# Kernel optimization log

Measured on AMD Instinct MI355X. Metric: run time of the kernel, lower is better.

The kernel has to match this reference:

```python
import jax, jax.numpy as jnp
import numpy as np

LAMBDA_SOFTMAX = 9.0
LAMBDA_LSE = 6.0
MARGIN = 0.2
EPS = 1e-8


def setup_inputs() -> dict:
    key = jax.random.key(0)
    k1, k2 = jax.random.split(key)
    im = jax.random.normal(k1, (128, 36, 1024), dtype=jnp.float32)
    s = jax.random.normal(k2, (128, 32, 1024), dtype=jnp.float32)
    return {"im": im, "s": s}


def _xattn_scores_t2i(im, s):
    # im: (n_image=J, n_region=R, D); s: (n_caption=I, n_word=W, D)
    # raw attention: context(image regions) x query(caption words)
    attn = jnp.einsum('jrd,iwd->ijrw', im, s)              # (I,J,R,W)
    # clipped_l2norm: LeakyReLU(0.1) then L2-normalize over word axis (dim=2 of (B,R,W))
    attn = jnp.where(attn > 0, attn, 0.1 * attn)
    norm = jnp.sqrt(jnp.sum(attn * attn, axis=3, keepdims=True)) + EPS
    attn = attn / norm
    # transpose to (I,J,W,R), softmax over regions with smoothing
    attn = jax.nn.softmax(LAMBDA_SOFTMAX * jnp.swapaxes(attn, 2, 3), axis=3)
    # weighted context per word: (I,J,W,D)
    wctx = jnp.einsum('ijwr,jrd->ijwd', attn, im)
    # cosine similarity between caption words and weighted image context, over D
    num = jnp.einsum('iwd,ijwd->ijw', s, wctx)
    w1 = jnp.linalg.norm(s, axis=2)                        # (I,W)
    w2 = jnp.linalg.norm(wctx, axis=3)                     # (I,J,W)
    sim = num / jnp.clip(w1[:, None, :] * w2, EPS, None)   # (I,J,W)
    # LogSumExp aggregation over words
    row = jax.nn.logsumexp(LAMBDA_LSE * sim, axis=2) / LAMBDA_LSE  # (I,J)
    # original stacks row_sim (n_image,1) along dim=1 -> scores[j, i]
    return row.T                                           # (n_image, n_caption)


def reference(im, s):
    scores = _xattn_scores_t2i(im, s)                      # (B,B)
    diag = jnp.diagonal(scores)
    cost_s = jnp.clip(MARGIN + scores - diag[:, None], 0.0, None)
    cost_im = jnp.clip(MARGIN + scores - diag[None, :], 0.0, None)
    mask = jnp.eye(scores.shape[0], dtype=bool)
    cost_s = jnp.where(mask, 0.0, cost_s)
    cost_im = jnp.where(mask, 0.0, cost_im)
    # max_violation = True
    return jnp.max(cost_s, axis=1).sum() + jnp.max(cost_im, axis=0).sum()
```

## Files before the change

### kernel.cpp

```cpp
#include <hip/hip_runtime.h>

#define NJ 128
#define NI 128
#define NR 36
#define NW 32
#define ND 1024

#define LAM_SM 9.0f
#define LAM_LSE 6.0f
#define MARGIN 0.2f
#define EPSF 1e-8f

typedef __attribute__((ext_vector_type(8))) short s16x8;
typedef __attribute__((ext_vector_type(4))) float f32x4;

#define IM_ROWS (NJ * NR)
#define S_ROWS  (NI * NW)
#define ALL_ROWS (IM_ROWS + S_ROWS)
#define IM_ELEMS (IM_ROWS * ND)
#define S_ELEMS  (S_ROWS * ND)
#define GSW_ELEMS (NJ * 48 * 64)

#define G_BOFF 36864
#define G_BUFSZ 69632
#define G_SMEM 139264
#define GRAM_SMEM 98304

__device__ __forceinline__ unsigned short f2bf(float x) {
    unsigned u = __float_as_uint(x);
    return (unsigned short)((u + 0x7FFFu + ((u >> 16) & 1u)) >> 16);
}
__device__ __forceinline__ unsigned pack2bf(float x, float y) {
    return (unsigned)f2bf(x) | ((unsigned)f2bf(y) << 16);
}
__device__ __forceinline__ float bf2f(unsigned v) {
    return __uint_as_float((v & 0xffffu) << 16);
}
__device__ __forceinline__ void gload16(const void* g, void* l) {
    __builtin_amdgcn_global_load_lds((const __attribute__((address_space(1))) unsigned int*)g,
                                     (__attribute__((address_space(3))) unsigned int*)l, 16, 0, 0);
}

__global__ __launch_bounds__(256) void cvtswz2_kernel(const float* __restrict__ im,
                                                      const float* __restrict__ s,
                                                      unsigned short* __restrict__ dst,
                                                      float* __restrict__ w1) {
    __shared__ float part[4];
    const int tid = threadIdx.x;
    int idx = blockIdx.x * 256 + tid;
    int row = idx >> 7, cw = idx & 127;
    int wd = cw >> 3, p = cw & 7;
    int sk = wd * 64 + ((p ^ (row & 7)) * 8);
    const float* srow = (row < IM_ROWS) ? (im + (size_t)row * ND)
                                        : (s + (size_t)(row - IM_ROWS) * ND);
    float4 v0 = *(const float4*)(srow + sk);
    float4 v1 = *(const float4*)(srow + sk + 4);
    ushort4 o0, o1;
    o0.x = f2bf(v0.x); o0.y = f2bf(v0.y); o0.z = f2bf(v0.z); o0.w = f2bf(v0.w);
    o1.x = f2bf(v1.x); o1.y = f2bf(v1.y); o1.z = f2bf(v1.z); o1.w = f2bf(v1.w);
    ((ushort4*)dst)[(size_t)idx * 2] = o0;
    ((ushort4*)dst)[(size_t)idx * 2 + 1] = o1;
    float ss = v0.x * v0.x + v0.y * v0.y + v0.z * v0.z + v0.w * v0.w +
               v1.x * v1.x + v1.y * v1.y + v1.z * v1.z + v1.w * v1.w;
    ss += __shfl_xor(ss, 1);  ss += __shfl_xor(ss, 2);  ss += __shfl_xor(ss, 4);
    ss += __shfl_xor(ss, 8);  ss += __shfl_xor(ss, 16); ss += __shfl_xor(ss, 32);
    if ((tid & 63) == 0) part[tid >> 6] = ss;
    __syncthreads();
    if ((tid & 127) == 0 && row >= IM_ROWS) {
        int h = tid >> 7;
        w1[row - IM_ROWS] = sqrtf(part[h * 2] + part[h * 2 + 1]);
    }
}

__global__ __launch_bounds__(512) void gram4_kernel(const unsigned short* __restrict__ imsw,
                                                    unsigned short* __restrict__ Gsw) {
    extern __shared__ char gsm[];
    const int j = blockIdx.x;
    const int tid = threadIdx.x;
    const int wv = tid >> 6, l = tid & 63;
    const int grp = l >> 4, lw = l & 15;
    char* reg = gsm + wv * 12288;

#pragma unroll
    for (int u = 0; u < 3; ++u)
        *(int4*)(reg + 36 * 256 + (l + u * 64) * 16) = make_int4(0, 0, 0, 0);
    {
        const char* src = (const char*)imsw + ((size_t)j * 36 + (l >> 4)) * 2048 +
                          wv * 256 + (l & 15) * 16;
#pragma unroll
        for (int c = 0; c < 9; ++c)
            gload16(src + (size_t)c * 4 * 2048, reg + c * 1024);
    }
    asm volatile("s_waitcnt vmcnt(0)" ::: "memory");

    const int keyadj = (j & 1) * 4;
    f32x4 acc[3][3];
#pragma unroll
    for (int m = 0; m < 3; ++m)
#pragma unroll
        for (int n = 0; n < 3; ++n) acc[m][n] = (f32x4){0.f, 0.f, 0.f, 0.f};

#pragma unroll
    for (int ks = 0; ks < 4; ++ks) {
        s16x8 fr[3];
#pragma unroll
        for (int m = 0; m < 3; ++m) {
            int r = m * 16 + lw;
            int swzg = ((((ks & 1) * 4 + grp) ^ ((r + keyadj) & 7)) << 4);
            fr[m] = *(const s16x8*)(reg + r * 256 + (ks >> 1) * 128 + swzg);
        }
#pragma unroll
        for (int m = 0; m < 3; ++m)
#pragma unroll
            for (int n = 0; n < 3; ++n)
                acc[m][n] = __builtin_amdgcn_mfma_f32_16x16x32_bf16(fr[m], fr[n], acc[m][n], 0, 0, 0);
    }
    __syncthreads();
    float* Gt = (float*)(gsm + wv * 9984);
#pragma unroll
    for (int m = 0; m < 3; ++m)
#pragma unroll
        for (int n = 0; n < 3; ++n)
#pragma unroll
            for (int r4 = 0; r4 < 4; ++r4)
                Gt[(m * 16 + grp * 4 + r4) * 52 + n * 16 + lw] = acc[m][n][r4];
    __syncthreads();
    if (tid < 384) {
        int row = tid >> 3, p = tid & 7;
        int k0 = (p ^ (row & 7)) * 8;
        float v[8];
#pragma unroll
        for (int i = 0; i < 8; ++i) {
            int k = k0 + i;
            float sum = 0.f;
            if (k < 48) {
#pragma unroll
                for (int w8 = 0; w8 < 8; ++w8)
                    sum += ((const float*)(gsm + w8 * 9984))[row * 52 + k];
            }
            v[i] = sum;
        }
        ushort4 o0, o1;
        o0.x = f2bf(v[0]); o0.y = f2bf(v[1]); o0.z = f2bf(v[2]); o0.w = f2bf(v[3]);
        o1.x = f2bf(v[4]); o1.y = f2bf(v[5]); o1.z = f2bf(v[6]); o1.w = f2bf(v[7]);
        ushort4* dp = (ushort4*)((char*)Gsw + (size_t)j * 6144 + row * 128 + p * 16);
        dp[0] = o0; dp[1] = o1;
    }
}

__global__ __attribute__((amdgpu_flat_work_group_size(512, 512)))
__attribute__((amdgpu_waves_per_eu(2, 2)))
void pairG_kernel(const unsigned short* __restrict__ imsw,
                  const unsigned short* __restrict__ ssw,
                  unsigned* __restrict__ C) {
    extern __shared__ char smem[];
    const int ig = blockIdx.x;
    const int jg = blockIdx.y;
    const int tid = threadIdx.x;
    const int l = tid & 63, wv = tid >> 6;
    const int grp = l >> 4, lw = l & 15;
    const int wm = wv >> 2, wn = wv & 3;

    const char* aSrc = (const char*)imsw + ((size_t)(jg * 288) + (l >> 3)) * 2048 + (l & 7) * 16;
    const char* bSrc = (const char*)ssw + ((size_t)(ig * 256) + (l >> 3)) * 2048 + (l & 7) * 16;

    f32x4 acc[9][4];
#pragma unroll
    for (int m = 0; m < 9; ++m)
#pragma unroll
        for (int n = 0; n < 4; ++n) acc[m][n] = (f32x4){0.f, 0.f, 0.f, 0.f};

    auto stage = [&](int bb, int k0b) {
        char* ab = smem + bb;
#pragma unroll
        for (int t = 0; t < 5; ++t) {
            int ii = wv + 8 * t;
            if (ii < 36) gload16(aSrc + (size_t)ii * 16384 + k0b, ab + ii * 1024);
        }
        char* bbp = smem + bb + G_BOFF;
#pragma unroll
        for (int t = 0; t < 4; ++t) {
            int ii = wv + 8 * t;
            gload16(bSrc + (size_t)ii * 16384 + k0b, bbp + ii * 1024);
        }
    };
    auto compute = [&](int bb) {
        const char* A = smem + bb;
        const char* B = smem + bb + G_BOFF;
#pragma unroll
        for (int ks = 0; ks < 2; ++ks) {
            const int swz = (((ks * 4 + grp) ^ (lw & 7)) << 4);
            s16x8 bf[4];
#pragma unroll
            for (int n = 0; n < 4; ++n)
                bf[n] = *(const s16x8*)(B + (wn * 64 + n * 16 + lw) * 128 + swz);
#pragma unroll
            for (int m = 0; m < 9; ++m) {
                s16x8 a = *(const s16x8*)(A + (wm * 144 + m * 16 + lw) * 128 + swz);
#pragma unroll
                for (int n = 0; n < 4; ++n)
                    acc[m][n] = __builtin_amdgcn_mfma_f32_16x16x32_bf16(a, bf[n], acc[m][n], 0, 0, 0);
            }
        }
    };

    stage(0, 0);
    asm volatile("s_waitcnt vmcnt(0)" ::: "memory");
    __syncthreads();
    for (int t = 0; t < 16; ++t) {
        if (t < 15) stage(((t + 1) & 1) * G_BUFSZ, (t + 1) * 128);
        compute((t & 1) * G_BUFSZ);
        asm volatile("s_waitcnt vmcnt(0)" ::: "memory");
        __syncthreads();
    }

#pragma unroll
    for (int L = 0; L < 4; ++L)
#pragma unroll
        for (int mm3 = 0; mm3 < 3; ++mm3) {
            const int m = 2 * L + mm3;
#pragma unroll
            for (int n = 0; n < 4; ++n) {
                const int p = (jg * 8 + wm * 4 + L) * NI + ig * 8 + wn * 2 + (n >> 1);
                const int nn = n & 1;
                size_t idx = ((size_t)(p * 3 + mm3) * 2 + nn) * 128 + l * 2;
                uint2 v;
                v.x = pack2bf(acc[m][n][0], acc[m][n][1]);
                v.y = pack2bf(acc[m][n][2], acc[m][n][3]);
                *(uint2*)(C + idx) = v;
            }
        }
}

__global__ __launch_bounds__(512) void pairE_kernel(const unsigned* __restrict__ C,
                                                    const unsigned short* __restrict__ Gswp,
                                                    const float* __restrict__ w1g,
                                                    float* __restrict__ scores) {
    __shared__ __align__(16) char smem[38912];
    const int ib = blockIdx.x;
    const int j = blockIdx.y;
    const int tid = threadIdx.x;
    const int l = tid & 63, wv = tid >> 6;
    const int grp = l >> 4, lw = l & 15;
    const int i = ib * 8 + wv;
    const int p = j * NI + i;
    const int L = j & 3;
    char* const Gd = smem;
    char* const myE = smem + 6144 + wv * 4096;

    if (tid < 384)
        *(int4*)(Gd + tid * 16) = *(const int4*)((const char*)Gswp + (size_t)j * 6144 + tid * 16);

    uint2 cv[3][2];
#pragma unroll
    for (int mm3 = 0; mm3 < 3; ++mm3)
#pragma unroll
        for (int nn = 0; nn < 2; ++nn)
            cv[mm3][nn] = *(const uint2*)(C + ((size_t)(p * 3 + mm3) * 2 + nn) * 128 + l * 2);

#pragma unroll
    for (int u = 0; u < 7; ++u) {
        int e = l + u * 64;
        int w = e / 14, pr = e - w * 14 + 18;
        *(unsigned*)(myE + w * 128 + (((pr >> 2) ^ (w & 7)) << 4) + (pr & 3) * 4) = 0u;
    }

#define AV(mm3, nn, reg) ((reg) == 0 ? bf2f(cv[mm3][nn].x) : (reg) == 1 ? bf2f(cv[mm3][nn].x >> 16) \
                          : (reg) == 2 ? bf2f(cv[mm3][nn].y) : bf2f(cv[mm3][nn].y >> 16))

    float inv[3][4];
#pragma unroll
    for (int mm3 = 0; mm3 < 3; ++mm3)
#pragma unroll
        for (int reg = 0; reg < 4; ++reg) {
            float a0 = AV(mm3, 0, reg), a1 = AV(mm3, 1, reg);
            float l0 = a0 > 0.f ? a0 : 0.1f * a0;
            float l1 = a1 > 0.f ? a1 : 0.1f * a1;
            float ss = l0 * l0 + l1 * l1;
            ss += __shfl_xor(ss, 1); ss += __shfl_xor(ss, 2);
            ss += __shfl_xor(ss, 4); ss += __shfl_xor(ss, 8);
            inv[mm3][reg] = 1.f / (sqrtf(ss) + EPSF);
        }

    float mx[2] = {-1e30f, -1e30f};
#pragma unroll
    for (int mm3 = 0; mm3 < 3; ++mm3) {
        int rbase = (2 * L + mm3) * 16 + grp * 4;
        bool pred = ((rbase * 1821) >> 16) == L;
#pragma unroll
        for (int nn = 0; nn < 2; ++nn) {
            float t4 = -1e30f;
#pragma unroll
            for (int reg = 0; reg < 4; ++reg) {
                float a = AV(mm3, nn, reg);
                float lk = a > 0.f ? a : 0.1f * a;
                t4 = fmaxf(t4, LAM_SM * lk * inv[mm3][reg]);
            }
            mx[nn] = pred ? fmaxf(mx[nn], t4) : mx[nn];
        }
    }
#pragma unroll
    for (int nn = 0; nn < 2; ++nn) {
        mx[nn] = fmaxf(mx[nn], __shfl_xor(mx[nn], 16));
        mx[nn] = fmaxf(mx[nn], __shfl_xor(mx[nn], 32));
    }

    float dn[2] = {0.f, 0.f}, nm[2] = {0.f, 0.f};
#pragma unroll
    for (int mm3 = 0; mm3 < 3; ++mm3) {
        int rbase = (2 * L + mm3) * 16 + grp * 4;
        bool pred = ((rbase * 1821) >> 16) == L;
        int rl0 = rbase - 36 * L;
#pragma unroll
        for (int nn = 0; nn < 2; ++nn) {
            int w = nn * 16 + lw;
            float e[4];
#pragma unroll
            for (int reg = 0; reg < 4; ++reg) {
                float a = AV(mm3, nn, reg);
                float lk = a > 0.f ? a : 0.1f * a;
                float tl = LAM_SM * lk * inv[mm3][reg];
                e[reg] = pred ? __expf(tl - mx[nn]) : 0.f;
                dn[nn] += e[reg];
                nm[nn] += e[reg] * a;
            }
            if (pred) {
                char* base = myE + w * 128 + (((rl0 >> 3) ^ (w & 7)) << 4) + (rl0 & 7) * 2;
                *(unsigned*)(base) = pack2bf(e[0], e[1]);
                *(unsigned*)(base + 4) = pack2bf(e[2], e[3]);
            }
        }
    }
#pragma unroll
    for (int nn = 0; nn < 2; ++nn) {
        dn[nn] += __shfl_xor(dn[nn], 16); dn[nn] += __shfl_xor(dn[nn], 32);
        nm[nn] += __shfl_xor(nm[nn], 16); nm[nn] += __shfl_xor(nm[nn], 32);
    }
    __syncthreads();

    f32x4 u[3][2];
#pragma unroll
    for (int m = 0; m < 3; ++m)
#pragma unroll
        for (int nn = 0; nn < 2; ++nn) u[m][nn] = (f32x4){0.f, 0.f, 0.f, 0.f};
#pragma unroll
    for (int ks = 0; ks < 2; ++ks) {
        int sz2 = (((ks * 4 + grp) ^ (lw & 7)) << 4);
        s16x8 ga[3], eb[2];
#pragma unroll
        for (int m = 0; m < 3; ++m)
            ga[m] = *(const s16x8*)(Gd + (m * 16 + lw) * 128 + sz2);
#pragma unroll
        for (int nn = 0; nn < 2; ++nn) {
            int w = nn * 16 + lw;
            eb[nn] = *(const s16x8*)(myE + w * 128 + (((ks * 4 + grp) ^ (w & 7)) << 4));
        }
#pragma unroll
        for (int m = 0; m < 3; ++m)
#pragma unroll
            for (int nn = 0; nn < 2; ++nn)
                u[m][nn] = __builtin_amdgcn_mfma_f32_16x16x32_bf16(ga[m], eb[nn], u[m][nn], 0, 0, 0);
    }
    float qq[2] = {0.f, 0.f};
#pragma unroll
    for (int m = 0; m < 3; ++m)
#pragma unroll
        for (int nn = 0; nn < 2; ++nn) {
            int w = nn * 16 + lw;
            const char* base = myE + w * 128;
#pragma unroll
            for (int rg = 0; rg < 4; rg += 2) {
                int rp = m * 16 + grp * 4 + rg;
                unsigned pv = *(const unsigned*)(base + (((rp >> 3) ^ (w & 7)) << 4) + (rp & 7) * 2);
                qq[nn] += u[m][nn][rg] * bf2f(pv) + u[m][nn][rg + 1] * bf2f(pv >> 16);
            }
        }
#pragma unroll
    for (int nn = 0; nn < 2; ++nn) {
        qq[nn] += __shfl_xor(qq[nn], 16); qq[nn] += __shfl_xor(qq[nn], 32);
    }
    float w1a = w1g[i * 32 + lw], w1b = w1g[i * 32 + 16 + lw];
    float s0 = nm[0] / fmaxf(w1a * sqrtf(fmaxf(qq[0], 0.f)), EPSF * dn[0]);
    float s1 = nm[1] / fmaxf(w1b * sqrtf(fmaxf(qq[1], 0.f)), EPSF * dn[1]);
    float m2 = fmaxf(s0, s1);
    m2 = fmaxf(m2, __shfl_xor(m2, 1)); m2 = fmaxf(m2, __shfl_xor(m2, 2));
    m2 = fmaxf(m2, __shfl_xor(m2, 4)); m2 = fmaxf(m2, __shfl_xor(m2, 8));
    float ssum = __expf(LAM_LSE * (s0 - m2)) + __expf(LAM_LSE * (s1 - m2));
    ssum += __shfl_xor(ssum, 1); ssum += __shfl_xor(ssum, 2);
    ssum += __shfl_xor(ssum, 4); ssum += __shfl_xor(ssum, 8);
    if (l == 0) scores[p] = m2 + logf(ssum) / LAM_LSE;
#undef AV
}

__global__ __launch_bounds__(1024) void loss_kernel(const float* __restrict__ scores,
                                                    float* __restrict__ out) {
    __shared__ float diag[NJ];
    __shared__ float part[1024];
    __shared__ float red[256];
    const int tid = threadIdx.x;
    if (tid < NJ) diag[tid] = scores[tid * NI + tid];
    __syncthreads();
    const int unit = tid >> 2, q = tid & 3;
    float m = 0.f;
    if (unit < 128) {
        const int a = unit;
        const float da = diag[a];
        for (int k = 0; k < 32; ++k) {
            int b = q * 32 + k;
            float c = MARGIN + scores[a * NI + b] - da;
            if (b != a) m = fmaxf(m, c);
        }
    } else {
        const int b = unit - 128;
        const float db = diag[b];
        for (int k = 0; k < 32; ++k) {
            int a = q * 32 + k;
            float c = MARGIN + scores[a * NI + b] - db;
            if (a != b) m = fmaxf(m, c);
        }
    }
    part[tid] = m;
    __syncthreads();
    if (q == 0)
        red[unit] = fmaxf(fmaxf(part[tid], part[tid + 1]), fmaxf(part[tid + 2], part[tid + 3]));
    __syncthreads();
    for (int st = 128; st > 0; st >>= 1) {
        if (tid < st) red[tid] += red[tid + st];
        __syncthreads();
    }
    if (tid == 0) out[0] = red[0];
}

extern "C" void kernel_launch(void* const* d_in, const int* in_sizes, int n_in,
                              void* d_out, int out_size, void* d_ws, size_t ws_size,
                              hipStream_t stream) {
    const float* im = (const float*)d_in[0];
    const float* s = (const float*)d_in[1];

    unsigned short* imsw = (unsigned short*)d_ws;
    unsigned short* ssw = imsw + IM_ELEMS;
    unsigned short* Gswp = ssw + S_ELEMS;
    float* w1 = (float*)(Gswp + GSW_ELEMS);
    float* scores = w1 + S_ROWS;
    unsigned* C = (unsigned*)(scores + NJ * NI);

    hipFuncSetAttribute((const void*)pairG_kernel,
                        hipFuncAttributeMaxDynamicSharedMemorySize, G_SMEM);
    hipFuncSetAttribute((const void*)gram4_kernel,
                        hipFuncAttributeMaxDynamicSharedMemorySize, GRAM_SMEM);

    cvtswz2_kernel<<<dim3(ALL_ROWS / 2), dim3(256), 0, stream>>>(im, s, imsw, w1);
    gram4_kernel<<<dim3(NJ), dim3(512), GRAM_SMEM, stream>>>(imsw, Gswp);
    pairG_kernel<<<dim3(NI / 8, NJ / 8), dim3(512), G_SMEM, stream>>>(imsw, ssw, C);
    pairE_kernel<<<dim3(NI / 8, NJ), dim3(512), 0, stream>>>(C, Gswp, w1, scores);
    loss_kernel<<<dim3(1), dim3(1024), 0, stream>>>(scores, (float*)d_out);
}
```

Before: 99.06 us.

## Replace double-buffered K pipeline with single-buffered 256-wide K tiles

The pairwise GEMM kernel drops its double-buffered 128-element K stages (16 iterations with prefetch overlapped with compute). It now uses a single LDS buffer holding 256-element K tiles, loading and computing them in 8 iterations. This halves the number of barriers and loop iterations and changes the global-to-LDS load mapping to 16 lanes per row. In exchange, loads no longer overlap with MFMA compute, so each iteration stalls on memory latency unless occupancy hides it.

```diff
diff --git a/kernel.cpp b/kernel.cpp
--- a/kernel.cpp
+++ b/kernel.cpp
@@ -21,8 +21,7 @@
 #define S_ELEMS  (S_ROWS * ND)
 #define GSW_ELEMS (NJ * 48 * 64)
 
-#define G_BOFF 36864
-#define G_BUFSZ 69632
+#define G_BOFF 73728
 #define G_SMEM 139264
 #define GRAM_SMEM 98304
 
@@ -161,8 +160,8 @@
     const int grp = l >> 4, lw = l & 15;
     const int wm = wv >> 2, wn = wv & 3;
 
-    const char* aSrc = (const char*)imsw + ((size_t)(jg * 288) + (l >> 3)) * 2048 + (l & 7) * 16;
-    const char* bSrc = (const char*)ssw + ((size_t)(ig * 256) + (l >> 3)) * 2048 + (l & 7) * 16;
+    const char* aSrc = (const char*)imsw + ((size_t)(jg * 288) + (l >> 4)) * 2048 + (l & 15) * 16;
+    const char* bSrc = (const char*)ssw + ((size_t)(ig * 256) + (l >> 4)) * 2048 + (l & 15) * 16;
 
     f32x4 acc[9][4];
 #pragma unroll
@@ -170,47 +169,34 @@
 #pragma unroll
         for (int n = 0; n < 4; ++n) acc[m][n] = (f32x4){0.f, 0.f, 0.f, 0.f};
 
-    auto stage = [&](int bb, int k0b) {
-        char* ab = smem + bb;
-#pragma unroll
-        for (int t = 0; t < 5; ++t) {
-            int ii = wv + 8 * t;
-            if (ii < 36) gload16(aSrc + (size_t)ii * 16384 + k0b, ab + ii * 1024);
-        }
-        char* bbp = smem + bb + G_BOFF;
-#pragma unroll
-        for (int t = 0; t < 4; ++t) {
-            int ii = wv + 8 * t;
-            gload16(bSrc + (size_t)ii * 16384 + k0b, bbp + ii * 1024);
-        }
-    };
-    auto compute = [&](int bb) {
-        const char* A = smem + bb;
-        const char* B = smem + bb + G_BOFF;
-#pragma unroll
-        for (int ks = 0; ks < 2; ++ks) {
-            const int swz = (((ks * 4 + grp) ^ (lw & 7)) << 4);
+    for (int t = 0; t < 8; ++t) {
+        const int k0b = t * 256;
+#pragma unroll
+        for (int u = 0; u < 17; ++u) {
+            int c = wv + 8 * u;
+            if (c < 72) gload16(aSrc + (size_t)c * 8192 + k0b, smem + c * 1024);
+            else if (c < 136) gload16(bSrc + (size_t)(c - 72) * 8192 + k0b,
+                                      smem + G_BOFF + (c - 72) * 1024);
+        }
+        asm volatile("s_waitcnt vmcnt(0)" ::: "memory");
+        __syncthreads();
+        const char* A = smem;
+        const char* B = smem + G_BOFF;
+#pragma unroll
+        for (int ks = 0; ks < 4; ++ks) {
+            const int off = (ks >> 1) * 128 + (((ks & 1) * 4 + grp) ^ (lw & 7)) * 16;
             s16x8 bf[4];
 #pragma unroll
             for (int n = 0; n < 4; ++n)
-                bf[n] = *(const s16x8*)(B + (wn * 64 + n * 16 + lw) * 128 + swz);
+                bf[n] = *(const s16x8*)(B + (wn * 64 + n * 16 + lw) * 256 + off);
 #pragma unroll
             for (int m = 0; m < 9; ++m) {
-                s16x8 a = *(const s16x8*)(A + (wm * 144 + m * 16 + lw) * 128 + swz);
+                s16x8 a = *(const s16x8*)(A + (wm * 144 + m * 16 + lw) * 256 + off);
 #pragma unroll
                 for (int n = 0; n < 4; ++n)
                     acc[m][n] = __builtin_amdgcn_mfma_f32_16x16x32_bf16(a, bf[n], acc[m][n], 0, 0, 0);
             }
         }
-    };
-
-    stage(0, 0);
-    asm volatile("s_waitcnt vmcnt(0)" ::: "memory");
-    __syncthreads();
-    for (int t = 0; t < 16; ++t) {
-        if (t < 15) stage(((t + 1) & 1) * G_BUFSZ, (t + 1) * 128);
-        compute((t & 1) * G_BUFSZ);
-        asm volatile("s_waitcnt vmcnt(0)" ::: "memory");
         __syncthreads();
     }
 
```

New measurement: 107.3 us. 1.08x slower.
